# Kernel optimization log

Hardware: AMD Instinct MI355X
Metric: run time of the kernel (lower is better)

The kernel has to match this reference:

```python
import jax, jax.numpy as jnp
import numpy as np
from jax import lax

N, G, L, D, E, STEPS = 65536, 128, 512, 128, 262144, 6
C = 2 * D  # concat dim (input_dim + output_dim)


def setup_inputs() -> dict:
    key = jax.random.key(0)
    ks = jax.random.split(key, 12)
    sD = 1.0 / float(np.sqrt(D))
    sC = 1.0 / float(np.sqrt(C))
    return {
        "x": jax.random.normal(ks[0], (N, D), jnp.float32),
        "edge_index": jax.random.randint(ks[1], (2, E), 0, N, dtype=jnp.int32),
        "edge_weight": jax.random.uniform(ks[2], (E,), jnp.float32),
        "batch": (jnp.arange(N) // L).astype(jnp.int32),  # sorted graph ids, L nodes/graph
        "ggnn_w": jax.random.normal(ks[3], (STEPS, D, D), jnp.float32) * sD,
        "gru_wih": jax.random.normal(ks[4], (3 * D, D), jnp.float32) * sD,
        "gru_whh": jax.random.normal(ks[5], (3 * D, D), jnp.float32) * sD,
        "gru_bih": jnp.zeros((3 * D,), jnp.float32),
        "gru_bhh": jnp.zeros((3 * D,), jnp.float32),
        "conv1_w": jax.random.normal(ks[6], (D, D, 3), jnp.float32) * sD,
        "conv1_b": jnp.zeros((D,), jnp.float32),
        "conv2_w": jax.random.normal(ks[7], (D, D, 1), jnp.float32) * sD,
        "conv2_b": jnp.zeros((D,), jnp.float32),
        "convc1_w": jax.random.normal(ks[8], (C, C, 3), jnp.float32) * sC,
        "convc1_b": jnp.zeros((C,), jnp.float32),
        "convc2_w": jax.random.normal(ks[9], (C, C, 1), jnp.float32) * sC,
        "convc2_b": jnp.zeros((C,), jnp.float32),
        "bn1_g": jnp.ones((D,), jnp.float32),
        "bn1_b": jnp.zeros((D,), jnp.float32),
        "bn2_g": jnp.ones((C,), jnp.float32),
        "bn2_b": jnp.zeros((C,), jnp.float32),
        "mlpy_w": jax.random.normal(ks[10], (2, D), jnp.float32) * sD,
        "mlpy_b": jnp.zeros((2,), jnp.float32),
        "mlpz_w": jax.random.normal(ks[11], (2, C), jnp.float32) * sC,
        "mlpz_b": jnp.zeros((2,), jnp.float32),
    }


def _gru(m, h, wih, whh, bih, bhh):
    gx = m @ wih.T + bih
    gh = h @ whh.T + bhh
    xr, xz, xn = jnp.split(gx, 3, axis=-1)
    hr, hz, hn = jnp.split(gh, 3, axis=-1)
    r = jax.nn.sigmoid(xr + hr)
    z = jax.nn.sigmoid(xz + hz)
    n = jnp.tanh(xn + r * hn)
    return (1.0 - z) * n + z * h


def _conv1d(x, w, b):  # x [G,Cin,L], w [Cout,Cin,K]
    y = lax.conv_general_dilated(x, w, (1,), "VALID", dimension_numbers=("NCH", "OIH", "NCH"))
    return y + b[None, :, None]


def _maxpool(x, k, s):
    return lax.reduce_window(x, -jnp.inf, lax.max, (1, 1, k), (1, 1, s), "VALID")


def _bn(x, g, b):  # training-mode BatchNorm1d over (N, L) per channel
    mean = x.mean(axis=(0, 2), keepdims=True)
    var = x.var(axis=(0, 2), keepdims=True)
    return (x - mean) * lax.rsqrt(var + 1e-5) * g[None, :, None] + b[None, :, None]


def reference(x, edge_index, edge_weight, batch, ggnn_w, gru_wih, gru_whh, gru_bih,
              gru_bhh, conv1_w, conv1_b, conv2_w, conv2_b, convc1_w, convc1_b,
              convc2_w, convc2_b, bn1_g, bn1_b, bn2_g, bn2_b, mlpy_w, mlpy_b,
              mlpz_w, mlpz_b):
    src, dst = edge_index[0], edge_index[1]

    # GatedGraphConv: per layer linear -> weighted message scatter-add -> GRU update
    def step(h, w):
        m = h @ w
        agg = jax.ops.segment_sum(m[src] * edge_weight[:, None], dst, num_segments=N)
        return _gru(agg, h, gru_wih, gru_whh, gru_bih, gru_bhh), None

    h, _ = lax.scan(step, x, ggnn_w)

    # de_batchify_graphs: one fused scatter into zero-padded [G, L, *] tensor
    counts = jax.ops.segment_sum(jnp.ones((N,), jnp.int32), batch, num_segments=G)
    offsets = jnp.cumsum(counts) - counts
    pos = jnp.arange(N) - offsets[batch]
    x_i = jnp.zeros((G, L, D), x.dtype).at[batch, pos].set(x)
    h_i = jnp.zeros((G, L, D), h.dtype).at[batch, pos].set(h)
    c_i = jnp.concatenate([h_i, x_i], axis=-1)  # [G, L, 2D]

    hT = h_i.transpose(0, 2, 1)  # [G, D, L]
    Y1 = _maxpool(jax.nn.relu(_bn(_conv1d(hT, conv1_w, conv1_b), bn1_g, bn1_b)), 3, 2)
    Y2 = _maxpool(jax.nn.relu(_bn(_conv1d(Y1, conv2_w, conv2_b), bn1_g, bn1_b)), 2, 2).transpose(0, 2, 1)
    cT = c_i.transpose(0, 2, 1)  # [G, 2D, L]
    Z1 = _maxpool(jax.nn.relu(_bn(_conv1d(cT, convc1_w, convc1_b), bn2_g, bn2_b)), 3, 2)
    Z2 = _maxpool(jax.nn.relu(_bn(_conv1d(Z1, convc2_w, convc2_b), bn2_g, bn2_b)), 2, 2).transpose(0, 2, 1)

    before_avg = (Y2 @ mlpy_w.T + mlpy_b) * (Z2 @ mlpz_w.T + mlpz_b)  # [G, L', 2]
    return before_avg.mean(axis=1)  # [G, 2]
```

## Files before the change

kernel.cpp:

```cpp
#include <hip/hip_runtime.h>
#include <math.h>

#define NN 65536
#define GG 128
#define LL 512
#define DD 128
#define EE 262144
#define NSTEPS 6
#define CC 256
#define L1 510
#define P1 254
#define P2 127

typedef __attribute__((ext_vector_type(8))) short s8bf;
typedef __attribute__((ext_vector_type(4))) float f4acc;

__device__ __forceinline__ unsigned short f2bf(float x) {
  unsigned u = __float_as_uint(x);
  unsigned r = u + 0x7FFFu + ((u >> 16) & 1u);
  return (unsigned short)(r >> 16);
}
__device__ __forceinline__ float bf2f(unsigned short h) {
  return __uint_as_float(((unsigned)h) << 16);
}
__device__ __forceinline__ unsigned short f2bf_sel(float x, int lo_sel) {
  unsigned short hi = f2bf(x);
  if (!lo_sel) return hi;
  return f2bf(x - bf2f(hi));
}
__device__ __forceinline__ uint2 pack4bf(float4 v, int lo_sel) {
  unsigned short s0 = f2bf_sel(v.x, lo_sel), s1 = f2bf_sel(v.y, lo_sel);
  unsigned short s2 = f2bf_sel(v.z, lo_sel), s3 = f2bf_sel(v.w, lo_sel);
  uint2 pk; pk.x = (unsigned)s0 | ((unsigned)s1 << 16);
  pk.y = (unsigned)s2 | ((unsigned)s3 << 16);
  return pk;
}

__global__ __launch_bounds__(256) void k_prep(
    const float* __restrict__ wih, const float* __restrict__ whh,
    const float* __restrict__ gw,
    const float* __restrict__ w1, const float* __restrict__ wc1,
    const float* __restrict__ w2, const float* __restrict__ wc2,
    unsigned short* __restrict__ wihCh, unsigned short* __restrict__ wihCl,
    unsigned short* __restrict__ whhCh, unsigned short* __restrict__ whhCl,
    unsigned short* __restrict__ gwTh, unsigned short* __restrict__ gwTl,
    unsigned short* __restrict__ c1h, unsigned short* __restrict__ c1l,
    unsigned short* __restrict__ cc1h, unsigned short* __restrict__ cc1l,
    unsigned short* __restrict__ c2h, unsigned short* __restrict__ c2l,
    unsigned short* __restrict__ cc2h, unsigned short* __restrict__ cc2l) {
  int i = blockIdx.x * 256 + threadIdx.x;
  if (i < 49152) {
    float v = wih[i];
    unsigned short h_ = f2bf(v);
    wihCh[i] = h_; wihCl[i] = f2bf(v - bf2f(h_));
    float u = whh[i];
    unsigned short h2 = f2bf(u);
    whhCh[i] = h2; whhCl[i] = f2bf(u - bf2f(h2));
  }
  if (i < 98304) {
    int s = i >> 14; int r = i & 16383; int c = r >> 7; int k = r & 127;
    float v = gw[(s << 14) + k * 128 + c];
    unsigned short h_ = f2bf(v);
    gwTh[i] = h_; gwTl[i] = f2bf(v - bf2f(h_));
  }
  if (i < 49152) {
    int ci = i & 127; int r = i >> 7; int co = r & 127; int tap = r >> 7;
    float v = w1[(co * 128 + ci) * 3 + tap];
    unsigned short h_ = f2bf(v);
    c1h[i] = h_; c1l[i] = f2bf(v - bf2f(h_));
  }
  if (i < 196608) {
    int ci = i & 255; int r = i >> 8; int co = r & 255; int tap = r >> 8;
    float v = wc1[(co * 256 + ci) * 3 + tap];
    unsigned short h_ = f2bf(v);
    cc1h[i] = h_; cc1l[i] = f2bf(v - bf2f(h_));
  }
  if (i < 16384) {
    float v = w2[i];
    unsigned short h_ = f2bf(v);
    c2h[i] = h_; c2l[i] = f2bf(v - bf2f(h_));
  }
  if (i < 65536) {
    float v = wc2[i];
    unsigned short h_ = f2bf(v);
    cc2h[i] = h_; cc2l[i] = f2bf(v - bf2f(h_));
  }
}

__global__ __launch_bounds__(256) void k_hist(const int* __restrict__ dst, int* __restrict__ cnt) {
  int e = blockIdx.x * 256 + threadIdx.x;
  if (e < EE) atomicAdd(&cnt[dst[e]], 1);
}

__global__ __launch_bounds__(1024) void k_scan(const int* __restrict__ cnt,
                                               int* __restrict__ rowptr,
                                               int* __restrict__ cursor) {
  __shared__ int part[1024];
  int t = threadIdx.x;
  int base = t * 64;
  int s = 0;
  for (int i = 0; i < 64; i++) s += cnt[base + i];
  part[t] = s;
  __syncthreads();
  for (int off = 1; off < 1024; off <<= 1) {
    int v = part[t];
    int u = (t >= off) ? part[t - off] : 0;
    __syncthreads();
    part[t] = v + u;
    __syncthreads();
  }
  int run = part[t] - s;
  for (int i = 0; i < 64; i++) {
    rowptr[base + i] = run;
    cursor[base + i] = run;
    run += cnt[base + i];
  }
  if (t == 1023) rowptr[NN] = run;
}

__global__ __launch_bounds__(256) void k_fill(const int* __restrict__ src,
                                              const int* __restrict__ dst,
                                              const float* __restrict__ ew,
                                              int* __restrict__ cursor,
                                              int* __restrict__ col,
                                              float* __restrict__ wgt) {
  int e = blockIdx.x * 256 + threadIdx.x;
  if (e < EE) {
    int d = dst[e];
    int p = atomicAdd(&cursor[d], 1);
    col[p] = src[e];
    wgt[p] = ew[e];
  }
}

__global__ __launch_bounds__(256, 4) void k_gemm_mfma(
    const float* __restrict__ A,
    const unsigned short* __restrict__ Wh, const unsigned short* __restrict__ Wl,
    float* __restrict__ Cout) {
  __shared__ __attribute__((aligned(16))) unsigned short As[64 * 136];
  int t = threadIdx.x;
  int r0 = blockIdx.x * 64;
  int wv = t >> 6, lane = t & 63;
  int ln = lane & 15, q = lane >> 4;
  f4acc acc[4][2];
#pragma unroll
  for (int mt = 0; mt < 4; mt++)
#pragma unroll
    for (int nt = 0; nt < 2; nt++) acc[mt][nt] = (f4acc)0.f;

  for (int p = 0; p < 3; p++) {
    if (p != 1) {
      const int a_lo = (p == 2);
      if (p) __syncthreads();
      for (int base = t * 4; base < 64 * 128; base += 1024) {
        int row = base >> 7, kk = base & 127;
        float4 v = *(const float4*)&A[(r0 + row) * 128 + kk];
        *(uint2*)&As[row * 136 + kk] = pack4bf(v, a_lo);
      }
      __syncthreads();
    }
    const unsigned short* W = (p == 1) ? Wl : Wh;
#pragma unroll
    for (int k0 = 0; k0 < 128; k0 += 32) {
      s8bf af[4], bf[2];
#pragma unroll
      for (int nt = 0; nt < 2; nt++)
        bf[nt] = *(const s8bf*)&W[(wv * 32 + nt * 16 + ln) * 128 + k0 + q * 8];
#pragma unroll
      for (int mt = 0; mt < 4; mt++)
        af[mt] = *(const s8bf*)&As[(mt * 16 + ln) * 136 + k0 + q * 8];
#pragma unroll
      for (int mt = 0; mt < 4; mt++)
#pragma unroll
        for (int nt = 0; nt < 2; nt++)
          acc[mt][nt] = __builtin_amdgcn_mfma_f32_16x16x32_bf16(af[mt], bf[nt], acc[mt][nt], 0, 0, 0);
    }
  }
#pragma unroll
  for (int mt = 0; mt < 4; mt++)
#pragma unroll
    for (int nt = 0; nt < 2; nt++)
#pragma unroll
      for (int reg = 0; reg < 4; reg++) {
        int r = r0 + mt * 16 + q * 4 + reg;
        Cout[r * 128 + wv * 32 + nt * 16 + ln] = acc[mt][nt][reg];
      }
}

__global__ __launch_bounds__(256) void k_gather(const float* __restrict__ m,
                                                const int* __restrict__ rowptr,
                                                const int* __restrict__ col,
                                                const float* __restrict__ wgt,
                                                float* __restrict__ agg) {
  int t = threadIdx.x;
  int n = blockIdx.x * 8 + (t >> 5);
  int c4 = t & 31;
  const float4* m4 = (const float4*)m;
  int s0 = rowptr[n], s1 = rowptr[n + 1];
  float ax = 0.f, ay = 0.f, az = 0.f, aw = 0.f;
  int e = s0;
  for (; e + 2 <= s1; e += 2) {
    int cA = col[e], cB = col[e + 1];
    float wA = wgt[e], wB = wgt[e + 1];
    float4 vA = m4[cA * 32 + c4];
    float4 vB = m4[cB * 32 + c4];
    ax += vA.x * wA + vB.x * wB;
    ay += vA.y * wA + vB.y * wB;
    az += vA.z * wA + vB.z * wB;
    aw += vA.w * wA + vB.w * wB;
  }
  if (e < s1) {
    int cA = col[e];
    float wA = wgt[e];
    float4 vA = m4[cA * 32 + c4];
    ax += vA.x * wA; ay += vA.y * wA; az += vA.z * wA; aw += vA.w * wA;
  }
  ((float4*)agg)[n * 32 + c4] = make_float4(ax, ay, az, aw);
}

__global__ __launch_bounds__(256, 2) void k_gru_mfma(
    const float* __restrict__ agg, const float* __restrict__ hin,
    const unsigned short* __restrict__ wihCh, const unsigned short* __restrict__ wihCl,
    const unsigned short* __restrict__ whhCh, const unsigned short* __restrict__ whhCl,
    const float* __restrict__ bih, const float* __restrict__ bhh,
    float* __restrict__ hout) {
  __shared__ __attribute__((aligned(16))) unsigned short As[2 * 64 * 136];
  int t = threadIdx.x;
  int r0 = blockIdx.x * 64;
  int d0 = blockIdx.y * 64;
  int wv = t >> 6, lane = t & 63;
  int ln = lane & 15, q = lane >> 4;
  f4acc acc[4][6];
#pragma unroll
  for (int mt = 0; mt < 4; mt++)
#pragma unroll
    for (int tg = 0; tg < 6; tg++) acc[mt][tg] = (f4acc)0.f;

  for (int p = 0; p < 3; p++) {
    if (p != 1) {
      const int a_lo = (p == 2);
      if (p) __syncthreads();
#pragma unroll
      for (int mat = 0; mat < 2; mat++) {
        const float* Asrc = mat ? hin : agg;
        for (int base = t * 4; base < 64 * 128; base += 1024) {
          int row = base >> 7, kk = base & 127;
          float4 v = *(const float4*)&Asrc[(r0 + row) * 128 + kk];
          *(uint2*)&As[mat * 8704 + row * 136 + kk] = pack4bf(v, a_lo);
        }
      }
      __syncthreads();
    }
    const unsigned short* wx = (p == 1) ? wihCl : wihCh;
    const unsigned short* wh = (p == 1) ? whhCl : whhCh;
#pragma unroll
    for (int k0 = 0; k0 < 128; k0 += 32) {
      s8bf af[2][4], bfr[6];
#pragma unroll
      for (int tg = 0; tg < 6; tg++) {
        int gate = (tg < 3) ? tg : tg - 3;
        const unsigned short* W = (tg < 3) ? wx : wh;
        bfr[tg] = *(const s8bf*)&W[(gate * 128 + d0 + wv * 16 + ln) * 128 + k0 + q * 8];
      }
#pragma unroll
      for (int mat = 0; mat < 2; mat++)
#pragma unroll
        for (int mt = 0; mt < 4; mt++)
          af[mat][mt] = *(const s8bf*)&As[mat * 8704 + (mt * 16 + ln) * 136 + k0 + q * 8];
#pragma unroll
      for (int mt = 0; mt < 4; mt++)
#pragma unroll
        for (int tg = 0; tg < 6; tg++)
          acc[mt][tg] = __builtin_amdgcn_mfma_f32_16x16x32_bf16(
              af[tg < 3 ? 0 : 1][mt], bfr[tg], acc[mt][tg], 0, 0, 0);
    }
  }
  int d = d0 + wv * 16 + ln;
  float bi0 = bih[d], bi1 = bih[128 + d], bi2 = bih[256 + d];
  float bh0 = bhh[d], bh1 = bhh[128 + d], bh2 = bhh[256 + d];
#pragma unroll
  for (int mt = 0; mt < 4; mt++) {
#pragma unroll
    for (int reg = 0; reg < 4; reg++) {
      int r = r0 + mt * 16 + q * 4 + reg;
      float hold = hin[r * 128 + d];
      float xr = acc[mt][0][reg] + bi0;
      float xz = acc[mt][1][reg] + bi1;
      float xn = acc[mt][2][reg] + bi2;
      float hr = acc[mt][3][reg] + bh0;
      float hz = acc[mt][4][reg] + bh1;
      float hn = acc[mt][5][reg] + bh2;
      float rr = 1.f / (1.f + expf(-(xr + hr)));
      float zz = 1.f / (1.f + expf(-(xz + hz)));
      float nnv = tanhf(xn + rr * hn);
      hout[r * 128 + d] = (1.f - zz) * nnv + zz * hold;
    }
  }
}

template<int CIN, int TAPS, int WA>
__global__ __launch_bounds__(256, 3) void k_conv_mfma(
    const float* __restrict__ inA, const float* __restrict__ inB,
    const unsigned short* __restrict__ Wh, const unsigned short* __restrict__ Wl,
    const float* __restrict__ bias, float* __restrict__ out,
    float* __restrict__ stats, int Lin, int Lco) {
  constexpr int APAD = CIN + 8;
  constexpr int ROWS = 64 + TAPS - 1;
  constexpr int NCH = CIN / 32;
  __shared__ __attribute__((aligned(16))) unsigned short As[ROWS * APAD];
  __shared__ float sred[256];
  const int g = blockIdx.z, co0 = blockIdx.y * 128, l0 = blockIdx.x * 64;
  const int t = threadIdx.x;
  const int wv = t >> 6, lane = t & 63, ln = lane & 15, q = lane >> 4;
  f4acc acc[4][2];
#pragma unroll
  for (int mt = 0; mt < 4; mt++)
#pragma unroll
    for (int nt = 0; nt < 2; nt++) acc[mt][nt] = (f4acc)0.f;

  for (int p = 0; p < 3; p++) {
    if (p != 1) {
      const int a_lo = (p == 2);
      if (p) __syncthreads();
      for (int base = t * 4; base < ROWS * CIN; base += 1024) {
        int row = base / CIN, ch = base % CIN;
        int lr = l0 + row; if (lr > Lin - 1) lr = Lin - 1;
        float4 v;
        if (ch < WA) v = *(const float4*)&inA[(g * Lin + lr) * WA + ch];
        else         v = *(const float4*)&inB[(g * Lin + lr) * WA + ch - WA];
        *(uint2*)&As[row * APAD + ch] = pack4bf(v, a_lo);
      }
      __syncthreads();
    }
    const unsigned short* W = (p == 1) ? Wl : Wh;
#pragma unroll
    for (int tap = 0; tap < TAPS; tap++) {
#pragma unroll
      for (int ch = 0; ch < NCH; ch++) {
        const int c0 = ch * 32;
        s8bf af[4], bf[2];
#pragma unroll
        for (int nt = 0; nt < 2; nt++)
          bf[nt] = *(const s8bf*)&W[(tap * CIN + co0 + wv * 32 + nt * 16 + ln) * CIN + c0 + q * 8];
#pragma unroll
        for (int mt = 0; mt < 4; mt++)
          af[mt] = *(const s8bf*)&As[(mt * 16 + ln + tap) * APAD + c0 + q * 8];
#pragma unroll
        for (int mt = 0; mt < 4; mt++)
#pragma unroll
          for (int nt = 0; nt < 2; nt++)
            acc[mt][nt] = __builtin_amdgcn_mfma_f32_16x16x32_bf16(af[mt], bf[nt], acc[mt][nt], 0, 0, 0);
      }
    }
  }
  sred[t] = 0.f;
  __syncthreads();
#pragma unroll
  for (int nt = 0; nt < 2; nt++) {
    int cl = wv * 32 + nt * 16 + ln;
    int co = co0 + cl;
    float bv = bias[co];
    float s = 0.f, s2 = 0.f;
#pragma unroll
    for (int mt = 0; mt < 4; mt++)
#pragma unroll
      for (int reg = 0; reg < 4; reg++) {
        int l = l0 + mt * 16 + q * 4 + reg;
        if (l < Lco) {
          float v = acc[mt][nt][reg] + bv;
          out[(g * Lco + l) * CIN + co] = v;
          s += v; s2 += v * v;
        }
      }
    atomicAdd(&sred[cl], s);
    atomicAdd(&sred[128 + cl], s2);
  }
  __syncthreads();
  if (t < 128) atomicAdd(&stats[co0 + t], sred[t]);
  else atomicAdd(&stats[CIN + co0 + (t - 128)], sred[t]);
}

__global__ __launch_bounds__(256) void k_bnpool(const float* __restrict__ in,
                                                float* __restrict__ out,
                                                const float* __restrict__ stats,
                                                const float* __restrict__ gamma,
                                                const float* __restrict__ beta,
                                                int Cch, int LinC, int Lout, int pk) {
  int idx = blockIdx.x * 256 + threadIdx.x;
  int total = GG * Cch * Lout;
  if (idx >= total) return;
  int c = idx & (Cch - 1);
  int r = idx / Cch;
  int p = r % Lout;
  int g = r / Lout;
  float cntf = (float)(GG * LinC);
  float mean = stats[c] / cntf;
  float var = stats[Cch + c] / cntf - mean * mean;
  float inv = rsqrtf(var + 1e-5f) * gamma[c];
  float sh = beta[c] - mean * inv;
  const float* base = &in[((g * LinC) + 2 * p) * Cch + c];
  float m = 0.f;
  for (int k = 0; k < pk; k++) {
    float v = fmaxf(base[k * Cch] * inv + sh, 0.f);
    m = fmaxf(m, v);
  }
  out[(g * Lout + p) * Cch + c] = m;
}

__global__ __launch_bounds__(128) void k_final(const float* __restrict__ Y2,
                                               const float* __restrict__ Z2,
                                               const float* __restrict__ myw,
                                               const float* __restrict__ myb,
                                               const float* __restrict__ mzw,
                                               const float* __restrict__ mzb,
                                               float* __restrict__ outp) {
  __shared__ float red0[128];
  __shared__ float red1[128];
  int g = blockIdx.x;
  int t = threadIdx.x;
  float y0 = myb[0], y1 = myb[1], z0 = mzb[0], z1 = mzb[1];
  if (t < P2) {
    const float* yb = &Y2[(g * P2 + t) * 128];
    for (int c = 0; c < 128; c++) {
      float v = yb[c];
      y0 += v * myw[c];
      y1 += v * myw[128 + c];
    }
    const float* zb = &Z2[(g * P2 + t) * 256];
    for (int c = 0; c < 256; c++) {
      float v = zb[c];
      z0 += v * mzw[c];
      z1 += v * mzw[256 + c];
    }
  }
  red0[t] = (t < P2) ? y0 * z0 : 0.f;
  red1[t] = (t < P2) ? y1 * z1 : 0.f;
  __syncthreads();
  for (int off = 64; off > 0; off >>= 1) {
    if (t < off) {
      red0[t] += red0[t + off];
      red1[t] += red1[t + off];
    }
    __syncthreads();
  }
  if (t == 0) {
    outp[g * 2 + 0] = red0[0] / 127.f;
    outp[g * 2 + 1] = red1[0] / 127.f;
  }
}

extern "C" void kernel_launch(void* const* d_in, const int* in_sizes, int n_in,
                              void* d_out, int out_size, void* d_ws, size_t ws_size,
                              hipStream_t stream) {
  const float* x   = (const float*)d_in[0];
  const int* ei    = (const int*)d_in[1];
  const float* ew  = (const float*)d_in[2];
  const float* gw  = (const float*)d_in[4];
  const float* wih = (const float*)d_in[5];
  const float* whh = (const float*)d_in[6];
  const float* bih = (const float*)d_in[7];
  const float* bhh = (const float*)d_in[8];
  const float* w1  = (const float*)d_in[9];
  const float* b1  = (const float*)d_in[10];
  const float* w2  = (const float*)d_in[11];
  const float* b2  = (const float*)d_in[12];
  const float* wc1 = (const float*)d_in[13];
  const float* bc1 = (const float*)d_in[14];
  const float* wc2 = (const float*)d_in[15];
  const float* bc2 = (const float*)d_in[16];
  const float* bn1g = (const float*)d_in[17];
  const float* bn1b = (const float*)d_in[18];
  const float* bn2g = (const float*)d_in[19];
  const float* bn2b = (const float*)d_in[20];
  const float* myw = (const float*)d_in[21];
  const float* myb = (const float*)d_in[22];
  const float* mzw = (const float*)d_in[23];
  const float* mzb = (const float*)d_in[24];
  float* out = (float*)d_out;

  float* ws   = (float*)d_ws;
  float* h    = ws;
  float* bufA = h + 8388608;
  float* bufB = bufA + 16711680;
  float* bufC = bufB + 8388608;
  float* Y2   = bufC + 8388608;
  float* Z2   = Y2 + 2080768;
  float* wslot = Z2 + 4161536;
  unsigned short* wihCh = (unsigned short*)wslot;
  unsigned short* wihCl = wihCh + 49152;
  unsigned short* whhCh = wihCl + 49152;
  unsigned short* whhCl = whhCh + 49152;
  unsigned short* c1h  = (unsigned short*)(wslot + 98304);
  unsigned short* c1l  = c1h + 49152;
  unsigned short* cc1h = c1l + 49152;
  unsigned short* cc1l = cc1h + 196608;
  unsigned short* c2h  = cc1l + 196608;
  unsigned short* c2l  = c2h + 16384;
  unsigned short* cc2h = c2l + 16384;
  unsigned short* cc2l = cc2h + 65536;
  float* stats = (float*)(cc2l + 65536);
  int* cnt    = (int*)(stats + 512);
  int* rowptr = cnt + 65536;
  int* cursor = rowptr + 65537;
  int* col    = cursor + 65536;
  float* wgt  = (float*)(col + 262144);
  unsigned short* gwTh = (unsigned short*)(wgt + 262144);
  unsigned short* gwTl = gwTh + 98304;
  size_t needed = (size_t)((float*)(gwTl + 98304) - ws) * 4;
  if (ws_size < needed) return;

  const int* src = ei;
  const int* dst = ei + EE;

  k_prep<<<768, 256, 0, stream>>>(wih, whh, gw, w1, wc1, w2, wc2,
                                  wihCh, wihCl, whhCh, whhCl, gwTh, gwTl,
                                  c1h, c1l, cc1h, cc1l, c2h, c2l, cc2h, cc2l);
  hipMemsetAsync(cnt, 0, 65536 * 4, stream);
  k_hist<<<1024, 256, 0, stream>>>(dst, cnt);
  k_scan<<<1, 1024, 0, stream>>>(cnt, rowptr, cursor);
  k_fill<<<1024, 256, 0, stream>>>(src, dst, ew, cursor, col, wgt);

  float* P = h;
  float* Q = bufC;
  float* m = bufA;
  float* agg = bufB;
  for (int s = 0; s < NSTEPS; s++) {
    const float* hcur = (s == 0) ? x : ((s & 1) ? Q : P);
    float* hnext = (s & 1) ? P : Q;
    k_gemm_mfma<<<1024, 256, 0, stream>>>(hcur, gwTh + s * 16384, gwTl + s * 16384, m);
    k_gather<<<8192, 256, 0, stream>>>(m, rowptr, col, wgt, agg);
    k_gru_mfma<<<dim3(1024, 2), 256, 0, stream>>>(agg, hcur, wihCh, wihCl,
                                                  whhCh, whhCl, bih, bhh, hnext);
  }

  hipMemsetAsync(stats, 0, 512 * 4, stream);
  k_conv_mfma<128, 3, 128><<<dim3(8, 1, 128), 256, 0, stream>>>(
      h, nullptr, c1h, c1l, b1, bufA, stats, 512, L1);
  k_bnpool<<<(GG * 128 * P1 + 255) / 256, 256, 0, stream>>>(bufA, bufB, stats, bn1g, bn1b, 128, L1, P1, 3);
  hipMemsetAsync(stats, 0, 512 * 4, stream);
  k_conv_mfma<128, 1, 128><<<dim3(4, 1, 128), 256, 0, stream>>>(
      bufB, nullptr, c2h, c2l, b2, bufC, stats, P1, P1);
  k_bnpool<<<(GG * 128 * P2 + 255) / 256, 256, 0, stream>>>(bufC, Y2, stats, bn1g, bn1b, 128, P1, P2, 2);

  hipMemsetAsync(stats, 0, 512 * 4, stream);
  k_conv_mfma<256, 3, 128><<<dim3(8, 2, 128), 256, 0, stream>>>(
      h, x, cc1h, cc1l, bc1, bufA, stats, 512, L1);
  k_bnpool<<<(GG * 256 * P1 + 255) / 256, 256, 0, stream>>>(bufA, bufB, stats, bn2g, bn2b, 256, L1, P1, 3);
  hipMemsetAsync(stats, 0, 512 * 4, stream);
  k_conv_mfma<256, 1, 256><<<dim3(4, 2, 128), 256, 0, stream>>>(
      bufB, nullptr, cc2h, cc2l, bc2, bufC, stats, P1, P1);
  k_bnpool<<<(GG * 256 * P2 + 255) / 256, 256, 0, stream>>>(bufC, Z2, stats, bn2g, bn2b, 256, P1, P2, 2);

  k_final<<<128, 128, 0, stream>>>(Y2, Z2, myw, myb, mzw, mzb, out);
}
```

Measured before the change: 1.647 ms.

## Store activations as pre-split bf16 hi/lo pairs instead of fp32

Producers (the GRU, the gather and the bn/pool stage, plus a new x-split kernel) now write activations as separate bf16 high and low halves rather than fp32. The GEMM, GRU and conv kernels then read these directly as MFMA operands, so the per-block fp32-to-bf16 split and its LDS staging and barriers go away in the GEMM and GRU. This cuts global read bytes and conversion ALU work. In exchange the producers do more conversion work, the GEMM and GRU fetch operands straight from global memory without shared-memory reuse, the conv launch bound is raised, and the conv branches are reordered to reuse buffers.

```diff
diff --git a/kernel.cpp b/kernel.cpp
--- a/kernel.cpp
+++ b/kernel.cpp
@@ -22,18 +22,6 @@
 }
 __device__ __forceinline__ float bf2f(unsigned short h) {
   return __uint_as_float(((unsigned)h) << 16);
-}
-__device__ __forceinline__ unsigned short f2bf_sel(float x, int lo_sel) {
-  unsigned short hi = f2bf(x);
-  if (!lo_sel) return hi;
-  return f2bf(x - bf2f(hi));
-}
-__device__ __forceinline__ uint2 pack4bf(float4 v, int lo_sel) {
-  unsigned short s0 = f2bf_sel(v.x, lo_sel), s1 = f2bf_sel(v.y, lo_sel);
-  unsigned short s2 = f2bf_sel(v.z, lo_sel), s3 = f2bf_sel(v.w, lo_sel);
-  uint2 pk; pk.x = (unsigned)s0 | ((unsigned)s1 << 16);
-  pk.y = (unsigned)s2 | ((unsigned)s3 << 16);
-  return pk;
 }
 
 __global__ __launch_bounds__(256) void k_prep(
@@ -87,6 +75,22 @@
   }
 }
 
+__global__ __launch_bounds__(256) void k_xsplit(const float* __restrict__ src,
+                                                unsigned short* __restrict__ dh,
+                                                unsigned short* __restrict__ dl) {
+  int i = (blockIdx.x * 256 + threadIdx.x) * 4;
+  float4 v = *(const float4*)&src[i];
+  unsigned short hx = f2bf(v.x), hy = f2bf(v.y), hz = f2bf(v.z), hw = f2bf(v.w);
+  uint2 hp; hp.x = (unsigned)hx | ((unsigned)hy << 16);
+  hp.y = (unsigned)hz | ((unsigned)hw << 16);
+  *(uint2*)&dh[i] = hp;
+  unsigned short lx = f2bf(v.x - bf2f(hx)), ly = f2bf(v.y - bf2f(hy));
+  unsigned short lz = f2bf(v.z - bf2f(hz)), lw = f2bf(v.w - bf2f(hw));
+  uint2 lp; lp.x = (unsigned)lx | ((unsigned)ly << 16);
+  lp.y = (unsigned)lz | ((unsigned)lw << 16);
+  *(uint2*)&dl[i] = lp;
+}
+
 __global__ __launch_bounds__(256) void k_hist(const int* __restrict__ dst, int* __restrict__ cnt) {
   int e = blockIdx.x * 256 + threadIdx.x;
   if (e < EE) atomicAdd(&cnt[dst[e]], 1);
@@ -134,10 +138,9 @@
 }
 
 __global__ __launch_bounds__(256, 4) void k_gemm_mfma(
-    const float* __restrict__ A,
+    const unsigned short* __restrict__ AH, const unsigned short* __restrict__ AL,
     const unsigned short* __restrict__ Wh, const unsigned short* __restrict__ Wl,
     float* __restrict__ Cout) {
-  __shared__ __attribute__((aligned(16))) unsigned short As[64 * 136];
   int t = threadIdx.x;
   int r0 = blockIdx.x * 64;
   int wv = t >> 6, lane = t & 63;
@@ -149,16 +152,7 @@
     for (int nt = 0; nt < 2; nt++) acc[mt][nt] = (f4acc)0.f;
 
   for (int p = 0; p < 3; p++) {
-    if (p != 1) {
-      const int a_lo = (p == 2);
-      if (p) __syncthreads();
-      for (int base = t * 4; base < 64 * 128; base += 1024) {
-        int row = base >> 7, kk = base & 127;
-        float4 v = *(const float4*)&A[(r0 + row) * 128 + kk];
-        *(uint2*)&As[row * 136 + kk] = pack4bf(v, a_lo);
-      }
-      __syncthreads();
-    }
+    const unsigned short* A = (p == 2) ? AL : AH;
     const unsigned short* W = (p == 1) ? Wl : Wh;
 #pragma unroll
     for (int k0 = 0; k0 < 128; k0 += 32) {
@@ -168,7 +162,7 @@
         bf[nt] = *(const s8bf*)&W[(wv * 32 + nt * 16 + ln) * 128 + k0 + q * 8];
 #pragma unroll
       for (int mt = 0; mt < 4; mt++)
-        af[mt] = *(const s8bf*)&As[(mt * 16 + ln) * 136 + k0 + q * 8];
+        af[mt] = *(const s8bf*)&A[(r0 + mt * 16 + ln) * 128 + k0 + q * 8];
 #pragma unroll
       for (int mt = 0; mt < 4; mt++)
 #pragma unroll
@@ -191,7 +185,8 @@
                                                 const int* __restrict__ rowptr,
                                                 const int* __restrict__ col,
                                                 const float* __restrict__ wgt,
-                                                float* __restrict__ agg) {
+                                                unsigned short* __restrict__ aggH,
+                                                unsigned short* __restrict__ aggL) {
   int t = threadIdx.x;
   int n = blockIdx.x * 8 + (t >> 5);
   int c4 = t & 31;
@@ -215,16 +210,25 @@
     float4 vA = m4[cA * 32 + c4];
     ax += vA.x * wA; ay += vA.y * wA; az += vA.z * wA; aw += vA.w * wA;
   }
-  ((float4*)agg)[n * 32 + c4] = make_float4(ax, ay, az, aw);
+  int base = n * 128 + c4 * 4;
+  unsigned short hx = f2bf(ax), hy = f2bf(ay), hz = f2bf(az), hw = f2bf(aw);
+  uint2 hp; hp.x = (unsigned)hx | ((unsigned)hy << 16);
+  hp.y = (unsigned)hz | ((unsigned)hw << 16);
+  *(uint2*)&aggH[base] = hp;
+  unsigned short lx = f2bf(ax - bf2f(hx)), ly = f2bf(ay - bf2f(hy));
+  unsigned short lz = f2bf(az - bf2f(hz)), lw = f2bf(aw - bf2f(hw));
+  uint2 lp; lp.x = (unsigned)lx | ((unsigned)ly << 16);
+  lp.y = (unsigned)lz | ((unsigned)lw << 16);
+  *(uint2*)&aggL[base] = lp;
 }
 
 __global__ __launch_bounds__(256, 2) void k_gru_mfma(
-    const float* __restrict__ agg, const float* __restrict__ hin,
+    const unsigned short* __restrict__ aggH, const unsigned short* __restrict__ aggL,
+    const unsigned short* __restrict__ hH, const unsigned short* __restrict__ hL,
     const unsigned short* __restrict__ wihCh, const unsigned short* __restrict__ wihCl,
     const unsigned short* __restrict__ whhCh, const unsigned short* __restrict__ whhCl,
     const float* __restrict__ bih, const float* __restrict__ bhh,
-    float* __restrict__ hout) {
-  __shared__ __attribute__((aligned(16))) unsigned short As[2 * 64 * 136];
+    unsigned short* __restrict__ outH, unsigned short* __restrict__ outL) {
   int t = threadIdx.x;
   int r0 = blockIdx.x * 64;
   int d0 = blockIdx.y * 64;
@@ -237,20 +241,8 @@
     for (int tg = 0; tg < 6; tg++) acc[mt][tg] = (f4acc)0.f;
 
   for (int p = 0; p < 3; p++) {
-    if (p != 1) {
-      const int a_lo = (p == 2);
-      if (p) __syncthreads();
-#pragma unroll
-      for (int mat = 0; mat < 2; mat++) {
-        const float* Asrc = mat ? hin : agg;
-        for (int base = t * 4; base < 64 * 128; base += 1024) {
-          int row = base >> 7, kk = base & 127;
-          float4 v = *(const float4*)&Asrc[(r0 + row) * 128 + kk];
-          *(uint2*)&As[mat * 8704 + row * 136 + kk] = pack4bf(v, a_lo);
-        }
-      }
-      __syncthreads();
-    }
+    const unsigned short* aA = (p == 2) ? aggL : aggH;
+    const unsigned short* hA = (p == 2) ? hL : hH;
     const unsigned short* wx = (p == 1) ? wihCl : wihCh;
     const unsigned short* wh = (p == 1) ? whhCl : whhCh;
 #pragma unroll
@@ -263,10 +255,10 @@
         bfr[tg] = *(const s8bf*)&W[(gate * 128 + d0 + wv * 16 + ln) * 128 + k0 + q * 8];
       }
 #pragma unroll
-      for (int mat = 0; mat < 2; mat++)
-#pragma unroll
-        for (int mt = 0; mt < 4; mt++)
-          af[mat][mt] = *(const s8bf*)&As[mat * 8704 + (mt * 16 + ln) * 136 + k0 + q * 8];
+      for (int mt = 0; mt < 4; mt++) {
+        af[0][mt] = *(const s8bf*)&aA[(r0 + mt * 16 + ln) * 128 + k0 + q * 8];
+        af[1][mt] = *(const s8bf*)&hA[(r0 + mt * 16 + ln) * 128 + k0 + q * 8];
+      }
 #pragma unroll
       for (int mt = 0; mt < 4; mt++)
 #pragma unroll
@@ -283,7 +275,7 @@
 #pragma unroll
     for (int reg = 0; reg < 4; reg++) {
       int r = r0 + mt * 16 + q * 4 + reg;
-      float hold = hin[r * 128 + d];
+      float hold = bf2f(hH[r * 128 + d]) + bf2f(hL[r * 128 + d]);
       float xr = acc[mt][0][reg] + bi0;
       float xz = acc[mt][1][reg] + bi1;
       float xn = acc[mt][2][reg] + bi2;
@@ -293,14 +285,18 @@
       float rr = 1.f / (1.f + expf(-(xr + hr)));
       float zz = 1.f / (1.f + expf(-(xz + hz)));
       float nnv = tanhf(xn + rr * hn);
-      hout[r * 128 + d] = (1.f - zz) * nnv + zz * hold;
+      float val = (1.f - zz) * nnv + zz * hold;
+      unsigned short hi = f2bf(val);
+      outH[r * 128 + d] = hi;
+      outL[r * 128 + d] = f2bf(val - bf2f(hi));
     }
   }
 }
 
 template<int CIN, int TAPS, int WA>
-__global__ __launch_bounds__(256, 3) void k_conv_mfma(
-    const float* __restrict__ inA, const float* __restrict__ inB,
+__global__ __launch_bounds__(256, 4) void k_conv_mfma(
+    const unsigned short* __restrict__ inAh, const unsigned short* __restrict__ inAl,
+    const unsigned short* __restrict__ inBh, const unsigned short* __restrict__ inBl,
     const unsigned short* __restrict__ Wh, const unsigned short* __restrict__ Wl,
     const float* __restrict__ bias, float* __restrict__ out,
     float* __restrict__ stats, int Lin, int Lco) {
@@ -320,15 +316,16 @@
 
   for (int p = 0; p < 3; p++) {
     if (p != 1) {
-      const int a_lo = (p == 2);
+      const unsigned short* pA = (p == 2) ? inAl : inAh;
+      const unsigned short* pB = (p == 2) ? inBl : inBh;
       if (p) __syncthreads();
-      for (int base = t * 4; base < ROWS * CIN; base += 1024) {
+      for (int base = t * 8; base < ROWS * CIN; base += 2048) {
         int row = base / CIN, ch = base % CIN;
         int lr = l0 + row; if (lr > Lin - 1) lr = Lin - 1;
-        float4 v;
-        if (ch < WA) v = *(const float4*)&inA[(g * Lin + lr) * WA + ch];
-        else         v = *(const float4*)&inB[(g * Lin + lr) * WA + ch - WA];
-        *(uint2*)&As[row * APAD + ch] = pack4bf(v, a_lo);
+        uint4 v;
+        if (ch < WA) v = *(const uint4*)&pA[(g * Lin + lr) * WA + ch];
+        else         v = *(const uint4*)&pB[(g * Lin + lr) * WA + ch - WA];
+        *(uint4*)&As[row * APAD + ch] = v;
       }
       __syncthreads();
     }
@@ -381,7 +378,9 @@
 }
 
 __global__ __launch_bounds__(256) void k_bnpool(const float* __restrict__ in,
-                                                float* __restrict__ out,
+                                                float* __restrict__ outF,
+                                                unsigned short* __restrict__ outH,
+                                                unsigned short* __restrict__ outL,
                                                 const float* __restrict__ stats,
                                                 const float* __restrict__ gamma,
                                                 const float* __restrict__ beta,
@@ -404,7 +403,14 @@
     float v = fmaxf(base[k * Cch] * inv + sh, 0.f);
     m = fmaxf(m, v);
   }
-  out[(g * Lout + p) * Cch + c] = m;
+  int oidx = (g * Lout + p) * Cch + c;
+  if (outH) {
+    unsigned short hi = f2bf(m);
+    outH[oidx] = hi;
+    outL[oidx] = f2bf(m - bf2f(hi));
+  } else {
+    outF[oidx] = m;
+  }
 }
 
 __global__ __launch_bounds__(128) void k_final(const float* __restrict__ Y2,
@@ -478,13 +484,13 @@
   const float* mzb = (const float*)d_in[24];
   float* out = (float*)d_out;
 
-  float* ws   = (float*)d_ws;
-  float* h    = ws;
-  float* bufA = h + 8388608;
-  float* bufB = bufA + 16711680;
-  float* bufC = bufB + 8388608;
-  float* Y2   = bufC + 8388608;
-  float* Z2   = Y2 + 2080768;
+  float* ws    = (float*)d_ws;
+  float* slotP = ws;
+  float* bufA  = slotP + 8388608;
+  float* bufB  = bufA + 16711680;
+  float* bufC  = bufB + 8388608;
+  float* Y2    = bufC + 8388608;
+  float* Z2    = Y2 + 2080768;
   float* wslot = Z2 + 4161536;
   unsigned short* wihCh = (unsigned short*)wslot;
   unsigned short* wihCl = wihCh + 49152;
@@ -509,6 +515,18 @@
   size_t needed = (size_t)((float*)(gwTl + 98304) - ws) * 4;
   if (ws_size < needed) return;
 
+  unsigned short* Ph = (unsigned short*)slotP;
+  unsigned short* Pl = Ph + 8388608;
+  unsigned short* Qh = (unsigned short*)bufC;
+  unsigned short* Ql = Qh + 8388608;
+  unsigned short* aggHp = (unsigned short*)bufB;
+  unsigned short* aggLp = aggHp + 8388608;
+  unsigned short* p1h = (unsigned short*)bufB;
+  unsigned short* p1l = p1h + 8323072;
+  float* m = bufA;
+  float* convOut = bufA;
+  float* c2out = bufC;
+
   const int* src = ei;
   const int* dst = ei + EE;
 
@@ -520,36 +538,43 @@
   k_scan<<<1, 1024, 0, stream>>>(cnt, rowptr, cursor);
   k_fill<<<1024, 256, 0, stream>>>(src, dst, ew, cursor, col, wgt);
 
-  float* P = h;
-  float* Q = bufC;
-  float* m = bufA;
-  float* agg = bufB;
+  k_xsplit<<<8192, 256, 0, stream>>>(x, Ph, Pl);
+
   for (int s = 0; s < NSTEPS; s++) {
-    const float* hcur = (s == 0) ? x : ((s & 1) ? Q : P);
-    float* hnext = (s & 1) ? P : Q;
-    k_gemm_mfma<<<1024, 256, 0, stream>>>(hcur, gwTh + s * 16384, gwTl + s * 16384, m);
-    k_gather<<<8192, 256, 0, stream>>>(m, rowptr, col, wgt, agg);
-    k_gru_mfma<<<dim3(1024, 2), 256, 0, stream>>>(agg, hcur, wihCh, wihCl,
-                                                  whhCh, whhCl, bih, bhh, hnext);
-  }
+    const unsigned short* inH = (s & 1) ? Qh : Ph;
+    const unsigned short* inL = (s & 1) ? Ql : Pl;
+    unsigned short* oH = (s & 1) ? Ph : Qh;
+    unsigned short* oL = (s & 1) ? Pl : Ql;
+    k_gemm_mfma<<<1024, 256, 0, stream>>>(inH, inL, gwTh + s * 16384, gwTl + s * 16384, m);
+    k_gather<<<8192, 256, 0, stream>>>(m, rowptr, col, wgt, aggHp, aggLp);
+    k_gru_mfma<<<dim3(1024, 2), 256, 0, stream>>>(aggHp, aggLp, inH, inL,
+                                                  wihCh, wihCl, whhCh, whhCl,
+                                                  bih, bhh, oH, oL);
+  }
+
+  k_xsplit<<<8192, 256, 0, stream>>>(x, Qh, Ql);
+
+  hipMemsetAsync(stats, 0, 512 * 4, stream);
+  k_conv_mfma<256, 3, 128><<<dim3(8, 2, 128), 256, 0, stream>>>(
+      Ph, Pl, Qh, Ql, cc1h, cc1l, bc1, convOut, stats, 512, L1);
+  k_bnpool<<<(GG * 256 * P1 + 255) / 256, 256, 0, stream>>>(
+      convOut, nullptr, p1h, p1l, stats, bn2g, bn2b, 256, L1, P1, 3);
+  hipMemsetAsync(stats, 0, 512 * 4, stream);
+  k_conv_mfma<256, 1, 256><<<dim3(4, 2, 128), 256, 0, stream>>>(
+      p1h, p1l, nullptr, nullptr, cc2h, cc2l, bc2, c2out, stats, P1, P1);
+  k_bnpool<<<(GG * 256 * P2 + 255) / 256, 256, 0, stream>>>(
+      c2out, Z2, nullptr, nullptr, stats, bn2g, bn2b, 256, P1, P2, 2);
 
   hipMemsetAsync(stats, 0, 512 * 4, stream);
   k_conv_mfma<128, 3, 128><<<dim3(8, 1, 128), 256, 0, stream>>>(
-      h, nullptr, c1h, c1l, b1, bufA, stats, 512, L1);
-  k_bnpool<<<(GG * 128 * P1 + 255) / 256, 256, 0, stream>>>(bufA, bufB, stats, bn1g, bn1b, 128, L1, P1, 3);
+      Ph, Pl, nullptr, nullptr, c1h, c1l, b1, convOut, stats, 512, L1);
+  k_bnpool<<<(GG * 128 * P1 + 255) / 256, 256, 0, stream>>>(
+      convOut, nullptr, p1h, p1l, stats, bn1g, bn1b, 128, L1, P1, 3);
   hipMemsetAsync(stats, 0, 512 * 4, stream);
   k_conv_mfma<128, 1, 128><<<dim3(4, 1, 128), 256, 0, stream>>>(
-      bufB, nullptr, c2h, c2l, b2, bufC, stats, P1, P1);
-  k_bnpool<<<(GG * 128 * P2 + 255) / 256, 256, 0, stream>>>(bufC, Y2, stats, bn1g, bn1b, 128, P1, P2, 2);
-
-  hipMemsetAsync(stats, 0, 512 * 4, stream);
-  k_conv_mfma<256, 3, 128><<<dim3(8, 2, 128), 256, 0, stream>>>(
-      h, x, cc1h, cc1l, bc1, bufA, stats, 512, L1);
-  k_bnpool<<<(GG * 256 * P1 + 255) / 256, 256, 0, stream>>>(bufA, bufB, stats, bn2g, bn2b, 256, L1, P1, 3);
-  hipMemsetAsync(stats, 0, 512 * 4, stream);
-  k_conv_mfma<256, 1, 256><<<dim3(4, 2, 128), 256, 0, stream>>>(
-      bufB, nullptr, cc2h, cc2l, bc2, bufC, stats, P1, P1);
-  k_bnpool<<<(GG * 256 * P2 + 255) / 256, 256, 0, stream>>>(bufC, Z2, stats, bn2g, bn2b, 256, P1, P2, 2);
+      p1h, p1l, nullptr, nullptr, c2h, c2l, b2, c2out, stats, P1, P1);
+  k_bnpool<<<(GG * 128 * P2 + 255) / 256, 256, 0, stream>>>(
+      c2out, Y2, nullptr, nullptr, stats, bn1g, bn1b, 128, P1, P2, 2);
 
   k_final<<<128, 128, 0, stream>>>(Y2, Z2, myw, myb, mzw, mzb, out);
 }
```

Result: slower. 2.031 ms (+23.3%).

## Pre-split conv inputs into bf16 hi/lo buffers and stage them directly

Applied to the files above, without the earlier changes.

Adds a k_xsplit kernel that converts the final hidden state and x into bf16 hi/lo halves once. The bnpool kernels also write bf16 hi/lo outputs for the intermediate conv inputs. The conv kernel now copies these with 16-byte loads straight into shared memory instead of loading fp32 and packing per tile, which cuts repeated conversion work and halves the bytes read on each staging pass. The launch bound rises to 4 blocks per SM, and the C-branch is reordered to run first so the workspace buffers can be reused. The cost is extra split passes and extra global writes, and the buffer aliasing must be exactly right.

```diff
diff --git a/kernel.cpp b/kernel.cpp
--- a/kernel.cpp
+++ b/kernel.cpp
@@ -85,6 +85,22 @@
     unsigned short h_ = f2bf(v);
     cc2h[i] = h_; cc2l[i] = f2bf(v - bf2f(h_));
   }
+}
+
+__global__ __launch_bounds__(256) void k_xsplit(const float* __restrict__ src,
+                                                unsigned short* __restrict__ dh,
+                                                unsigned short* __restrict__ dl) {
+  int i = (blockIdx.x * 256 + threadIdx.x) * 4;
+  float4 v = *(const float4*)&src[i];
+  unsigned short hx = f2bf(v.x), hy = f2bf(v.y), hz = f2bf(v.z), hw = f2bf(v.w);
+  uint2 hp; hp.x = (unsigned)hx | ((unsigned)hy << 16);
+  hp.y = (unsigned)hz | ((unsigned)hw << 16);
+  *(uint2*)&dh[i] = hp;
+  unsigned short lx = f2bf(v.x - bf2f(hx)), ly = f2bf(v.y - bf2f(hy));
+  unsigned short lz = f2bf(v.z - bf2f(hz)), lw = f2bf(v.w - bf2f(hw));
+  uint2 lp; lp.x = (unsigned)lx | ((unsigned)ly << 16);
+  lp.y = (unsigned)lz | ((unsigned)lw << 16);
+  *(uint2*)&dl[i] = lp;
 }
 
 __global__ __launch_bounds__(256) void k_hist(const int* __restrict__ dst, int* __restrict__ cnt) {
@@ -299,8 +315,9 @@
 }
 
 template<int CIN, int TAPS, int WA>
-__global__ __launch_bounds__(256, 3) void k_conv_mfma(
-    const float* __restrict__ inA, const float* __restrict__ inB,
+__global__ __launch_bounds__(256, 4) void k_conv_mfma(
+    const unsigned short* __restrict__ inAh, const unsigned short* __restrict__ inAl,
+    const unsigned short* __restrict__ inBh, const unsigned short* __restrict__ inBl,
     const unsigned short* __restrict__ Wh, const unsigned short* __restrict__ Wl,
     const float* __restrict__ bias, float* __restrict__ out,
     float* __restrict__ stats, int Lin, int Lco) {
@@ -320,15 +337,16 @@
 
   for (int p = 0; p < 3; p++) {
     if (p != 1) {
-      const int a_lo = (p == 2);
+      const unsigned short* pA = (p == 2) ? inAl : inAh;
+      const unsigned short* pB = (p == 2) ? inBl : inBh;
       if (p) __syncthreads();
-      for (int base = t * 4; base < ROWS * CIN; base += 1024) {
+      for (int base = t * 8; base < ROWS * CIN; base += 2048) {
         int row = base / CIN, ch = base % CIN;
         int lr = l0 + row; if (lr > Lin - 1) lr = Lin - 1;
-        float4 v;
-        if (ch < WA) v = *(const float4*)&inA[(g * Lin + lr) * WA + ch];
-        else         v = *(const float4*)&inB[(g * Lin + lr) * WA + ch - WA];
-        *(uint2*)&As[row * APAD + ch] = pack4bf(v, a_lo);
+        uint4 v;
+        if (ch < WA) v = *(const uint4*)&pA[(g * Lin + lr) * WA + ch];
+        else         v = *(const uint4*)&pB[(g * Lin + lr) * WA + ch - WA];
+        *(uint4*)&As[row * APAD + ch] = v;
       }
       __syncthreads();
     }
@@ -381,7 +399,9 @@
 }
 
 __global__ __launch_bounds__(256) void k_bnpool(const float* __restrict__ in,
-                                                float* __restrict__ out,
+                                                float* __restrict__ outF,
+                                                unsigned short* __restrict__ outH,
+                                                unsigned short* __restrict__ outL,
                                                 const float* __restrict__ stats,
                                                 const float* __restrict__ gamma,
                                                 const float* __restrict__ beta,
@@ -404,7 +424,14 @@
     float v = fmaxf(base[k * Cch] * inv + sh, 0.f);
     m = fmaxf(m, v);
   }
-  out[(g * Lout + p) * Cch + c] = m;
+  int oidx = (g * Lout + p) * Cch + c;
+  if (outH) {
+    unsigned short hi = f2bf(m);
+    outH[oidx] = hi;
+    outL[oidx] = f2bf(m - bf2f(hi));
+  } else {
+    outF[oidx] = m;
+  }
 }
 
 __global__ __launch_bounds__(128) void k_final(const float* __restrict__ Y2,
@@ -478,13 +505,13 @@
   const float* mzb = (const float*)d_in[24];
   float* out = (float*)d_out;
 
-  float* ws   = (float*)d_ws;
-  float* h    = ws;
-  float* bufA = h + 8388608;
-  float* bufB = bufA + 16711680;
-  float* bufC = bufB + 8388608;
-  float* Y2   = bufC + 8388608;
-  float* Z2   = Y2 + 2080768;
+  float* ws    = (float*)d_ws;
+  float* slotP = ws;
+  float* bufA  = slotP + 8388608;
+  float* bufB  = bufA + 16711680;
+  float* bufC  = bufB + 8388608;
+  float* Y2    = bufC + 8388608;
+  float* Z2    = Y2 + 2080768;
   float* wslot = Z2 + 4161536;
   unsigned short* wihCh = (unsigned short*)wslot;
   unsigned short* wihCl = wihCh + 49152;
@@ -509,6 +536,19 @@
   size_t needed = (size_t)((float*)(gwTl + 98304) - ws) * 4;
   if (ws_size < needed) return;
 
+  float* P = slotP;
+  float* Q = bufC;
+  float* m = bufA;
+  float* agg = bufB;
+  unsigned short* hPh = (unsigned short*)bufB;
+  unsigned short* hPl = hPh + 8388608;
+  unsigned short* xPh = (unsigned short*)bufC;
+  unsigned short* xPl = xPh + 8388608;
+  unsigned short* p1h = (unsigned short*)bufC;
+  unsigned short* p1l = p1h + 8323072;
+  float* convOut = bufA;
+  float* c2out = bufA;
+
   const int* src = ei;
   const int* dst = ei + EE;
 
@@ -520,10 +560,6 @@
   k_scan<<<1, 1024, 0, stream>>>(cnt, rowptr, cursor);
   k_fill<<<1024, 256, 0, stream>>>(src, dst, ew, cursor, col, wgt);
 
-  float* P = h;
-  float* Q = bufC;
-  float* m = bufA;
-  float* agg = bufB;
   for (int s = 0; s < NSTEPS; s++) {
     const float* hcur = (s == 0) ? x : ((s & 1) ? Q : P);
     float* hnext = (s & 1) ? P : Q;
@@ -533,23 +569,30 @@
                                                   whhCh, whhCl, bih, bhh, hnext);
   }
 
+  k_xsplit<<<8192, 256, 0, stream>>>(P, hPh, hPl);
+  k_xsplit<<<8192, 256, 0, stream>>>(x, xPh, xPl);
+
+  hipMemsetAsync(stats, 0, 512 * 4, stream);
+  k_conv_mfma<256, 3, 128><<<dim3(8, 2, 128), 256, 0, stream>>>(
+      hPh, hPl, xPh, xPl, cc1h, cc1l, bc1, convOut, stats, 512, L1);
+  k_bnpool<<<(GG * 256 * P1 + 255) / 256, 256, 0, stream>>>(
+      convOut, nullptr, p1h, p1l, stats, bn2g, bn2b, 256, L1, P1, 3);
+  hipMemsetAsync(stats, 0, 512 * 4, stream);
+  k_conv_mfma<256, 1, 256><<<dim3(4, 2, 128), 256, 0, stream>>>(
+      p1h, p1l, nullptr, nullptr, cc2h, cc2l, bc2, c2out, stats, P1, P1);
+  k_bnpool<<<(GG * 256 * P2 + 255) / 256, 256, 0, stream>>>(
+      c2out, Z2, nullptr, nullptr, stats, bn2g, bn2b, 256, P1, P2, 2);
+
   hipMemsetAsync(stats, 0, 512 * 4, stream);
   k_conv_mfma<128, 3, 128><<<dim3(8, 1, 128), 256, 0, stream>>>(
-      h, nullptr, c1h, c1l, b1, bufA, stats, 512, L1);
-  k_bnpool<<<(GG * 128 * P1 + 255) / 256, 256, 0, stream>>>(bufA, bufB, stats, bn1g, bn1b, 128, L1, P1, 3);
+      hPh, hPl, nullptr, nullptr, c1h, c1l, b1, convOut, stats, 512, L1);
+  k_bnpool<<<(GG * 128 * P1 + 255) / 256, 256, 0, stream>>>(
+      convOut, nullptr, p1h, p1l, stats, bn1g, bn1b, 128, L1, P1, 3);
   hipMemsetAsync(stats, 0, 512 * 4, stream);
   k_conv_mfma<128, 1, 128><<<dim3(4, 1, 128), 256, 0, stream>>>(
-      bufB, nullptr, c2h, c2l, b2, bufC, stats, P1, P1);
-  k_bnpool<<<(GG * 128 * P2 + 255) / 256, 256, 0, stream>>>(bufC, Y2, stats, bn1g, bn1b, 128, P1, P2, 2);
-
-  hipMemsetAsync(stats, 0, 512 * 4, stream);
-  k_conv_mfma<256, 3, 128><<<dim3(8, 2, 128), 256, 0, stream>>>(
-      h, x, cc1h, cc1l, bc1, bufA, stats, 512, L1);
-  k_bnpool<<<(GG * 256 * P1 + 255) / 256, 256, 0, stream>>>(bufA, bufB, stats, bn2g, bn2b, 256, L1, P1, 3);
-  hipMemsetAsync(stats, 0, 512 * 4, stream);
-  k_conv_mfma<256, 1, 256><<<dim3(4, 2, 128), 256, 0, stream>>>(
-      bufB, nullptr, cc2h, cc2l, bc2, bufC, stats, P1, P1);
-  k_bnpool<<<(GG * 256 * P2 + 255) / 256, 256, 0, stream>>>(bufC, Z2, stats, bn2g, bn2b, 256, P1, P2, 2);
+      p1h, p1l, nullptr, nullptr, c2h, c2l, b2, c2out, stats, P1, P1);
+  k_bnpool<<<(GG * 128 * P2 + 255) / 256, 256, 0, stream>>>(
+      c2out, Y2, nullptr, nullptr, stats, bn1g, bn1b, 128, P1, P2, 2);
 
   k_final<<<128, 128, 0, stream>>>(Y2, Z2, myw, myb, mzw, mzb, out);
 }
```

New measurement: 1.676 ms. No clear change (+1.7%).
